# Kernel tuning notes

Measured on AMD Instinct MI355X. Metric: run time of the kernel, lower is better.

Reference implementation:

```python
import jax, jax.numpy as jnp
import numpy as np
from jax import lax

HIDDEN = 64


def setup_inputs() -> dict:
    key = jax.random.key(0)
    ks = jax.random.split(key, 8)
    B, T, C, H, W = 8, 16, 3, 64, 64
    x = jax.random.normal(ks[0], (B, T, C, H, W), dtype=jnp.float32)
    # SE-style attention 1x1 convs (no bias): fc1 3->1, fc2 1->3
    att_w1 = jax.random.normal(ks[1], (1, 3), dtype=jnp.float32) * 0.5
    att_w2 = jax.random.normal(ks[2], (3, 1), dtype=jnp.float32) * 0.5
    # ConvLSTM layer 0: in = 3 + 64 = 67, out = 4*64 gates, 3x3 kernel
    conv_w0 = jax.random.normal(ks[3], (4 * HIDDEN, 3 + HIDDEN, 3, 3), dtype=jnp.float32) * 0.05
    conv_b0 = jnp.zeros((4 * HIDDEN,), dtype=jnp.float32)
    # ConvLSTM layer 1: in = 64 + 64 = 128
    conv_w1 = jax.random.normal(ks[4], (4 * HIDDEN, 2 * HIDDEN, 3, 3), dtype=jnp.float32) * 0.05
    conv_b1 = jnp.zeros((4 * HIDDEN,), dtype=jnp.float32)
    return {"x": x, "att_w1": att_w1, "att_w2": att_w2,
            "conv_w0": conv_w0, "conv_b0": conv_b0,
            "conv_w1": conv_w1, "conv_b1": conv_b1}


def _attention_scale(x, w1, w2):
    # x: [B, T, C, H, W] -> channel attention per timestep, vectorized over B,T
    avg = x.mean(axis=(-2, -1))          # [B, T, C]
    mx = x.max(axis=(-2, -1))            # [B, T, C]
    def fc(v):
        return jnp.einsum('or,btr->bto', w2, jax.nn.relu(jnp.einsum('rc,btc->btr', w1, v)))
    return jax.nn.sigmoid(fc(avg) + fc(mx))  # [B, T, C]


def _convlstm_layer(xseq, w, b, hidden):
    # xseq: [B, T, Cin, H, W]; returns ([B, T, hidden, H, W], h_last, c_last)
    B, T, Cin, H, W = xseq.shape
    h0 = jnp.zeros((B, hidden, H, W), xseq.dtype)
    c0 = jnp.zeros((B, hidden, H, W), xseq.dtype)

    def step(carry, xt):
        h, c = carry
        comb = jnp.concatenate([xt, h], axis=1)  # [B, Cin+hidden, H, W]
        conv = lax.conv_general_dilated(
            comb, w, window_strides=(1, 1), padding='SAME',
            dimension_numbers=('NCHW', 'OIHW', 'NCHW')) + b[None, :, None, None]
        cc_i, cc_f, cc_o, cc_g = jnp.split(conv, 4, axis=1)
        c_new = jax.nn.sigmoid(cc_f) * c + jax.nn.sigmoid(cc_i) * jnp.tanh(cc_g)
        h_new = jax.nn.sigmoid(cc_o) * jnp.tanh(c_new)
        return (h_new, c_new), h_new

    (h_last, c_last), hs = lax.scan(step, (h0, c0), jnp.moveaxis(xseq, 1, 0))
    return jnp.moveaxis(hs, 0, 1), h_last, c_last


def reference(x, att_w1, att_w2, conv_w0, conv_b0, conv_w1, conv_b1):
    # attention gating (broadcast [B,T,C,1,1] over H,W as in torch broadcast assign)
    scale = _attention_scale(x, att_w1, att_w2)
    xin = x * scale[..., None, None]
    out0, _, _ = _convlstm_layer(xin, conv_w0, conv_b0, HIDDEN)
    out1, h1, c1 = _convlstm_layer(out0, conv_w1, conv_b1, HIDDEN)
    # return_all_layers=False: last layer output + its final state
    return out1, h1, c1
```

## Files before the change

kernel.cpp:

```cpp
#include <hip/hip_runtime.h>
#include <hip/hip_bf16.h>
#include <math.h>

#define HW 4096
#define NB 8
#define NT 16

typedef unsigned short u16;
typedef __attribute__((ext_vector_type(8))) short bf16x8;
typedef __attribute__((ext_vector_type(4))) float f32x4;

__device__ __forceinline__ float sigmoid_f(float x) {
  return 1.f / (1.f + __expf(-x));
}
__device__ __forceinline__ float tanh_f(float x) {
  float ax = fabsf(x);
  float e = __expf(2.f * ax);
  float t = 1.f - 2.f / (e + 1.f);
  return copysignf(t, x);
}
__device__ __forceinline__ u16 f2b(float v) {
  __hip_bfloat16 h = __float2bfloat16(v);
  return *(u16*)&h;
}

__global__ void transform_wB(const float* __restrict__ w, u16* __restrict__ wtB,
                             int CIN, int cinbase, int nch) {
  int idx = blockIdx.x * 256 + threadIdx.x;
  int total = nch * 9 * 256 * 32;
  if (idx >= total) return;
  int ci32 = idx & 31;
  int rest = idx >> 5;
  int gate = rest & 255;
  rest >>= 8;
  int tap = rest % 9;
  int chunk = rest / 9;
  int cin = cinbase + chunk * 32 + ci32;
  wtB[idx] = f2b(w[((size_t)gate * CIN + cin) * 9 + tap]);
}

__global__ void transform_wA(const float* __restrict__ w0, u16* __restrict__ wtA) {
  int idx = blockIdx.x * 256 + threadIdx.x;
  if (idx >= 8192) return;
  int k = idx & 31, gate = idx >> 5;
  u16 v = 0;
  if (k < 27) {
    int ci = (k >= 18) + (k >= 9);
    int tap = k - ci * 9;
    v = f2b(w0[((size_t)gate * 67 + ci) * 9 + tap]);
  }
  wtA[idx] = v;
}

__global__ void att_reduce(const float* __restrict__ x, float* __restrict__ avg,
                           float* __restrict__ mx) {
  int btc = blockIdx.x;
  const float* p = x + (size_t)btc * HW;
  float s = 0.f, m = -INFINITY;
  for (int i = threadIdx.x; i < HW; i += 256) {
    float v = p[i];
    s += v;
    m = fmaxf(m, v);
  }
  #pragma unroll
  for (int off = 32; off; off >>= 1) {
    s += __shfl_down(s, off, 64);
    m = fmaxf(m, __shfl_down(m, off, 64));
  }
  __shared__ float ss[4], sm[4];
  int wid = threadIdx.x >> 6, lane = threadIdx.x & 63;
  if (lane == 0) { ss[wid] = s; sm[wid] = m; }
  __syncthreads();
  if (threadIdx.x == 0) {
    avg[btc] = (ss[0] + ss[1] + ss[2] + ss[3]) * (1.f / 4096.f);
    mx[btc]  = fmaxf(fmaxf(sm[0], sm[1]), fmaxf(sm[2], sm[3]));
  }
}

__global__ void att_apply(const float* __restrict__ x, const float* __restrict__ avg,
                          const float* __restrict__ mx, const float* __restrict__ w1,
                          const float* __restrict__ w2, u16* __restrict__ xin_t) {
  size_t i = (size_t)blockIdx.x * 256 + threadIdx.x;
  int pix = (int)(i & 4095);
  int c   = (int)((i >> 12) % 3);
  int bt  = (int)(i / (3 * HW));
  const float* a = avg + bt * 3;
  const float* m = mx + bt * 3;
  float ra = fmaxf(0.f, w1[0] * a[0] + w1[1] * a[1] + w1[2] * a[2]);
  float rm = fmaxf(0.f, w1[0] * m[0] + w1[1] * m[1] + w1[2] * m[2]);
  float sc = sigmoid_f(w2[c] * (ra + rm));
  xin_t[((size_t)bt * HW + pix) * 4 + c] = f2b(x[i] * sc);
}

struct RoleP {
  const u16* a0; long a0_bs; const u16* wtA;
  const u16* s0; long s0_bs; int s0_ch;
  const u16* s1; long s1_bs; int s1_ch;
  const u16* wtB; const float* bias;
  float* c_t;
  u16* h_t;
  float* out_f32; long out_bs;
};

__device__ __forceinline__ void dma_site(const u16* sp, u16* bufn, int idx,
                                         const u16* zb, int r0g) {
  int site = idx >> 2, sub = idx & 3;
  int r = site / 66, cc = site - r * 66;
  int gr = r0g - 1 + r, gc = cc - 1;
  const u16* g = (site < 264 && (unsigned)gr < 64u && (unsigned)gc < 64u)
               ? sp + (size_t)(gr * 64 + gc) * 32 + sub * 8
               : zb;
  u16* l = bufn + (size_t)(idx & ~63) * 8;
  __builtin_amdgcn_global_load_lds(
      (const __attribute__((address_space(1))) unsigned int*)g,
      (__attribute__((address_space(3))) unsigned int*)l, 16, 0, 0);
}

__device__ __forceinline__ void dma_chunk(const u16* sp, u16* bufn, const u16* zb,
                                          int r0g, int tid) {
  #pragma unroll
  for (int it = 0; it < 4; ++it) dma_site(sp, bufn, it * 256 + tid, zb, r0g);
  if (tid < 64) dma_site(sp, bufn, 1024 + tid, zb, r0g);
}

#define BQ_LOAD(S, BASE, TP)                                              \
  { _Pragma("unroll")                                                     \
    for (int _g = 0; _g < 4; ++_g)                                        \
      bq[S][_g] = *(const bf16x8*)((BASE) + (TP) * 8192 + _g * 2048); }

template <int PAR>
__device__ __forceinline__ void chunk_compute(const u16* bufc, const u16* bpc,
                                              const u16* bpn, bool more,
                                              bf16x8 (&bq)[2][4], f32x4 (&acc)[8][4],
                                              int abase) {
  #pragma unroll
  for (int tap = 0; tap < 9; ++tap) {
    if (tap < 8) { BQ_LOAD((tap + 1 + PAR) & 1, bpc, tap + 1) }
    else if (more) { BQ_LOAD((1 + PAR) & 1, bpn, 0) }
    const int dy = tap / 3, dx = tap - dy * 3;
    bf16x8 av[8];
    #pragma unroll
    for (int mt = 0; mt < 8; ++mt)
      av[mt] = *(const bf16x8*)(bufc + abase + ((mt >> 2) + dy) * 2112 + dx * 32 + (mt & 3) * 512);
    #pragma unroll
    for (int mt = 0; mt < 8; ++mt)
      #pragma unroll
      for (int gt = 0; gt < 4; ++gt)
        acc[mt][gt] = __builtin_amdgcn_mfma_f32_16x16x32_bf16(
            av[mt], bq[(tap + PAR) & 1][gt], acc[mt][gt], 0, 0, 0);
  }
}

#define SP_SET(CG)                                                           \
  sp = ((CG) < P.s0_ch)                                                      \
     ? P.s0 + (size_t)b * P.s0_bs + (size_t)(CG) * 131072                    \
     : P.s1 + (size_t)b * P.s1_bs + (size_t)((CG) - P.s0_ch) * 131072;

__global__ __launch_bounds__(256, 2) void conv_step(
    RoleP r0p, RoleP r1p, int zbase, const u16* __restrict__ zb)
{
  __shared__ __align__(16) u16 smem[2][8704];
  __shared__ __align__(16) u16 xtile[4096];
  const RoleP P = (blockIdx.z + zbase) ? r1p : r0p;
  const int r0g = blockIdx.x * 2, b = blockIdx.y;
  const int tid = threadIdx.x;
  const int gc = tid >> 6, lane = tid & 63;
  const int n = lane & 15, q = lane >> 4;
  const int abase = n * 32 + q * 8;
  const int ntot = P.s0_ch + P.s1_ch;

  f32x4 acc[8][4];
  #pragma unroll
  for (int mt = 0; mt < 8; ++mt)
    #pragma unroll
    for (int gt = 0; gt < 4; ++gt)
      acc[mt][gt] = (f32x4){0.f, 0.f, 0.f, 0.f};

  const u16* bp0 = P.wtB + (size_t)(gc * 16 + n) * 32 + q * 8;
  bf16x8 bq[2][4];
  const u16* sp;

  SP_SET(0);
  dma_chunk(sp, &smem[0][0], zb, r0g, tid);
  BQ_LOAD(0, bp0, 0)
  if (P.a0) {
    const u16* ap = P.a0 + (size_t)b * P.a0_bs;
    for (int idx = tid; idx < 4096; idx += 256) {
      int row = idx >> 11, rest = idx & 2047;
      int k = rest & 31, px = rest >> 5;
      u16 v = 0;
      if (k < 27) {
        int ci = (k >= 18) + (k >= 9);
        int tap = k - ci * 9;
        int dy = (tap >= 6) ? 2 : (tap >= 3 ? 1 : 0);
        int dx = tap - dy * 3;
        int gr = r0g + row - 1 + dy, gcl = px - 1 + dx;
        if ((unsigned)gr < 64u && (unsigned)gcl < 64u)
          v = ap[((size_t)(gr * 64 + gcl)) * 4 + ci];
      }
      xtile[idx] = v;
    }
  }
  __syncthreads();
  if (P.a0) {
    bf16x8 bxa[4], axv[8];
    #pragma unroll
    for (int gt = 0; gt < 4; ++gt)
      bxa[gt] = *(const bf16x8*)(P.wtA + ((gc + 4 * gt) * 16 + n) * 32 + q * 8);
    #pragma unroll
    for (int mt = 0; mt < 8; ++mt)
      axv[mt] = *(const bf16x8*)(xtile + (mt >> 2) * 2048 + ((mt & 3) * 16 + n) * 32 + q * 8);
    #pragma unroll
    for (int mt = 0; mt < 8; ++mt)
      #pragma unroll
      for (int gt = 0; gt < 4; ++gt)
        acc[mt][gt] = __builtin_amdgcn_mfma_f32_16x16x32_bf16(axv[mt], bxa[gt], acc[mt][gt], 0, 0, 0);
  }

  int cur = 0;
  for (int cg = 0; cg < ntot; cg += 2) {
    {
      SP_SET(cg + 1);
      dma_chunk(sp, &smem[cur ^ 1][0], zb, r0g, tid);
      chunk_compute<0>(&smem[cur][0], bp0 + (size_t)cg * 73728,
                       bp0 + (size_t)(cg + 1) * 73728, true, bq, acc, abase);
      __syncthreads();
      cur ^= 1;
    }
    {
      bool more = (cg + 2 < ntot);
      if (more) {
        SP_SET(cg + 2);
        dma_chunk(sp, &smem[cur ^ 1][0], zb, r0g, tid);
      }
      chunk_compute<1>(&smem[cur][0], bp0 + (size_t)(cg + 1) * 73728,
                       bp0 + (size_t)(cg + 2) * 73728, more, bq, acc, abase);
      __syncthreads();
      cur ^= 1;
    }
  }

  const int hc = gc * 16 + n;
  const float bi = P.bias[hc], bfv = P.bias[64 + hc], bo = P.bias[128 + hc], bg = P.bias[192 + hc];
  float* cB = P.c_t + ((size_t)b * HW + r0g * 64) * 64 + hc;
  u16*   hB = P.h_t + (size_t)b * 262144 + (size_t)(hc >> 5) * 131072
            + (size_t)(r0g * 64) * 32 + (hc & 31);
  float* tbuf = (float*)&smem[0][0];
  #pragma unroll
  for (int mt = 0; mt < 8; ++mt) {
    #pragma unroll
    for (int reg = 0; reg < 4; ++reg) {
      int px = mt * 16 + q * 4 + reg;
      float xi = acc[mt][0][reg] + bi;
      float xf = acc[mt][1][reg] + bfv;
      float xo = acc[mt][2][reg] + bo;
      float xg = acc[mt][3][reg] + bg;
      float ii = sigmoid_f(xi), ff = sigmoid_f(xf), oo = sigmoid_f(xo), gg = tanh_f(xg);
      float cold = cB[(size_t)px * 64];
      float cnew = ff * cold + ii * gg;
      float hnew = oo * tanh_f(cnew);
      cB[(size_t)px * 64] = cnew;
      hB[(size_t)px * 32] = f2b(hnew);
      if (P.out_f32) tbuf[px * 65 + hc] = hnew;
    }
  }
  if (P.out_f32) {
    __syncthreads();
    int hc2 = tid >> 2, qq = tid & 3;
    #pragma unroll
    for (int rw = 0; rw < 2; ++rw) {
      float* orow = P.out_f32 + (size_t)b * P.out_bs + (size_t)hc2 * HW + (r0g + rw) * 64;
      #pragma unroll
      for (int j = 0; j < 4; ++j) {
        int p0x = qq * 4 + j * 16;
        float4 v = make_float4(tbuf[(rw * 64 + p0x + 0) * 65 + hc2],
                               tbuf[(rw * 64 + p0x + 1) * 65 + hc2],
                               tbuf[(rw * 64 + p0x + 2) * 65 + hc2],
                               tbuf[(rw * 64 + p0x + 3) * 65 + hc2]);
        *(float4*)(orow + p0x) = v;
      }
    }
  }
}

__global__ void h1_final(const float* __restrict__ out1, float* __restrict__ dst) {
  size_t i = (size_t)blockIdx.x * 256 + threadIdx.x;
  size_t b = i >> 18, rem = i & 262143;
  dst[i] = out1[(b * NT + (NT - 1)) * 262144 + rem];
}

__global__ void c1_final(const float* __restrict__ c_t, float* __restrict__ dst) {
  __shared__ float t[64][65];
  int pb = blockIdx.x, b = blockIdx.y;
  int tx = threadIdx.x & 63, ty = threadIdx.x >> 6;
  for (int i = 0; i < 16; ++i) {
    int p = i * 4 + ty;
    t[p][tx] = c_t[((size_t)b * HW + pb * 64 + p) * 64 + tx];
  }
  __syncthreads();
  for (int i = 0; i < 16; ++i) {
    int hcv = i * 4 + ty;
    dst[(size_t)b * 262144 + (size_t)hcv * HW + pb * 64 + tx] = t[tx][hcv];
  }
}

extern "C" void kernel_launch(void* const* d_in, const int* in_sizes, int n_in,
                              void* d_out, int out_size, void* d_ws, size_t ws_size,
                              hipStream_t stream) {
  const float* x      = (const float*)d_in[0];
  const float* att_w1 = (const float*)d_in[1];
  const float* att_w2 = (const float*)d_in[2];
  const float* w0     = (const float*)d_in[3];
  const float* b0     = (const float*)d_in[4];
  const float* w1     = (const float*)d_in[5];
  const float* b1     = (const float*)d_in[6];
  float* out = (float*)d_out;
  char* ws = (char*)d_ws;

  u16*   xin_t = (u16*)(ws + 0);
  u16*   h0a   = (u16*)(ws + 4194304);
  u16*   h0b   = (u16*)(ws + 8388608);
  u16*   h1a   = (u16*)(ws + 12582912);
  u16*   h1b   = (u16*)(ws + 16777216);
  u16*   zb    = (u16*)(ws + 20971520);
  u16*   wtA0  = (u16*)(ws + 21495808);
  u16*   wtB0  = (u16*)(ws + 21512192);
  u16*   wtB1  = (u16*)(ws + 21807104);
  float* c0_t  = (float*)(ws + 22396928);
  float* c1_t  = (float*)(ws + 30785536);
  float* avg   = (float*)(ws + 39174144);
  float* mxb   = (float*)(ws + 39175680);
  if (ws_size < 39177216u) return;

  hipMemsetAsync(xin_t, 0, 4194304, stream);
  hipMemsetAsync(zb, 0, 524288, stream);
  hipMemsetAsync(c0_t, 0, 8388608, stream);
  hipMemsetAsync(c1_t, 0, 8388608, stream);

  transform_wA<<<32, 256, 0, stream>>>(w0, wtA0);
  transform_wB<<<576, 256, 0, stream>>>(w0, wtB0, 67, 3, 2);
  transform_wB<<<1152, 256, 0, stream>>>(w1, wtB1, 128, 0, 4);
  att_reduce<<<NB * NT * 3, 256, 0, stream>>>(x, avg, mxb);
  att_apply<<<1572864 / 256, 256, 0, stream>>>(x, avg, mxb, att_w1, att_w2, xin_t);

  const long HB = 262144;

  for (int s = 0; s <= NT; ++s) {
    bool has0 = (s < NT), has1 = (s > 0);
    RoleP p0 = {}, p1 = {};
    if (has0) {
      int t = s;
      p0.a0 = xin_t + (size_t)t * 16384; p0.a0_bs = (long)NT * 16384; p0.wtA = wtA0;
      p0.s0 = (t == 0) ? zb : ((t & 1) ? h0a : h0b);
      p0.s0_bs = (t == 0) ? 0L : HB; p0.s0_ch = 2;
      p0.s1 = zb; p0.s1_bs = 0L; p0.s1_ch = 0;
      p0.wtB = wtB0; p0.bias = b0; p0.c_t = c0_t;
      p0.h_t = (t & 1) ? h0b : h0a;
      p0.out_f32 = (float*)0; p0.out_bs = 0L;
    }
    if (has1) {
      int t = s - 1;
      p1.a0 = (const u16*)0; p1.a0_bs = 0L; p1.wtA = (const u16*)0;
      p1.s0 = (t & 1) ? h0b : h0a;
      p1.s0_bs = HB; p1.s0_ch = 2;
      p1.s1 = (t == 0) ? zb : ((t & 1) ? h1a : h1b);
      p1.s1_bs = (t == 0) ? 0L : HB; p1.s1_ch = 2;
      p1.wtB = wtB1; p1.bias = b1; p1.c_t = c1_t;
      p1.h_t = (t & 1) ? h1b : h1a;
      p1.out_f32 = out + (size_t)t * 262144; p1.out_bs = (long)NT * 262144;
    }
    int zbase = has0 ? 0 : 1;
    int zn = (has0 && has1) ? 2 : 1;
    conv_step<<<dim3(32, 8, zn), 256, 0, stream>>>(p0, p1, zbase, zb);
  }

  h1_final<<<8192, 256, 0, stream>>>(out, out + 33554432);
  c1_final<<<dim3(64, 8), 256, 0, stream>>>(c1_t, out + 35651584);
}
```

Measured before the change: 914.9 us.

## Replace per-step conv launches with a persistent kernel and grid barrier

The 17 separate conv_step launches, one per wavefront step of the two-layer ConvLSTM, are replaced by a single persistent kernel of 512 blocks. Each block keeps a fixed role (layer 0 or layer 1) and spatial tile, and the blocks synchronise between steps with an atomic-counter grid barrier. This is meant to remove kernel launch and drain gaps between steps. The barrier relies on all 512 blocks being co-resident (2 blocks per CU at 256 CUs), and its spin loop has a timeout that could silently break synchronisation.

```diff
diff --git a/kernel.cpp b/kernel.cpp
--- a/kernel.cpp
+++ b/kernel.cpp
@@ -5,6 +5,8 @@
 #define HW 4096
 #define NB 8
 #define NT 16
+#define HB 262144L
+#define NBLK 512
 
 typedef unsigned short u16;
 typedef __attribute__((ext_vector_type(8))) short bf16x8;
@@ -102,6 +104,14 @@
   float* out_f32; long out_bs;
 };
 
+struct PP {
+  const u16* xin; const u16* wtA;
+  const u16* wtB0; const float* b0; float* c0; u16* h0a; u16* h0b;
+  const u16* wtB1; const float* b1; float* c1; u16* h1a; u16* h1b;
+  const u16* zb; float* out;
+  unsigned* bar;
+};
+
 __device__ __forceinline__ void dma_site(const u16* sp, u16* bufn, int idx,
                                          const u16* zb, int r0g) {
   int site = idx >> 2, sub = idx & 3;
@@ -156,14 +166,9 @@
      ? P.s0 + (size_t)b * P.s0_bs + (size_t)(CG) * 131072                    \
      : P.s1 + (size_t)b * P.s1_bs + (size_t)((CG) - P.s0_ch) * 131072;
 
-__global__ __launch_bounds__(256, 2) void conv_step(
-    RoleP r0p, RoleP r1p, int zbase, const u16* __restrict__ zb)
-{
-  __shared__ __align__(16) u16 smem[2][8704];
-  __shared__ __align__(16) u16 xtile[4096];
-  const RoleP P = (blockIdx.z + zbase) ? r1p : r0p;
-  const int r0g = blockIdx.x * 2, b = blockIdx.y;
-  const int tid = threadIdx.x;
+__device__ __forceinline__ void conv_body(const RoleP& P, const u16* zb,
+                                          u16 (&smem)[2][8704], u16 (&xtile)[4096],
+                                          int r0g, int b, int tid) {
   const int gc = tid >> 6, lane = tid & 63;
   const int n = lane & 15, q = lane >> 4;
   const int abase = n * 32 + q * 8;
@@ -283,6 +288,65 @@
   }
 }
 
+__device__ __forceinline__ void grid_barrier(unsigned* bar, unsigned step) {
+  __syncthreads();
+  if (threadIdx.x == 0) {
+    __threadfence();
+    unsigned old = __hip_atomic_fetch_add(&bar[0], 1u, __ATOMIC_ACQ_REL,
+                                          __HIP_MEMORY_SCOPE_AGENT);
+    if (old == NBLK - 1u) {
+      __hip_atomic_store(&bar[0], 0u, __ATOMIC_RELAXED, __HIP_MEMORY_SCOPE_AGENT);
+      __hip_atomic_store(&bar[1], step + 1u, __ATOMIC_RELEASE, __HIP_MEMORY_SCOPE_AGENT);
+    } else {
+      long spins = 0;
+      while (__hip_atomic_load(&bar[1], __ATOMIC_ACQUIRE,
+                               __HIP_MEMORY_SCOPE_AGENT) <= step) {
+        __builtin_amdgcn_s_sleep(2);
+        if (++spins > 2000000L) break;
+      }
+    }
+    __threadfence();
+  }
+  __syncthreads();
+}
+
+__global__ __launch_bounds__(256, 2) void conv_persist(PP pp) {
+  __shared__ __align__(16) u16 smem[2][8704];
+  __shared__ __align__(16) u16 xtile[4096];
+  const int bid = blockIdx.x;
+  const int role = bid & 1, tile = bid >> 1;
+  const int r0g = (tile & 31) * 2, b = tile >> 5;
+  const int tid = threadIdx.x;
+
+  for (int s = 0; s <= NT; ++s) {
+    const bool active = role ? (s > 0) : (s < NT);
+    if (active) {
+      const int t = role ? (s - 1) : s;
+      RoleP P;
+      if (!role) {
+        P.a0 = pp.xin + (size_t)t * 16384; P.a0_bs = (long)NT * 16384; P.wtA = pp.wtA;
+        P.s0 = (t == 0) ? pp.zb : ((t & 1) ? pp.h0a : pp.h0b);
+        P.s0_bs = (t == 0) ? 0L : HB; P.s0_ch = 2;
+        P.s1 = pp.zb; P.s1_bs = 0L; P.s1_ch = 0;
+        P.wtB = pp.wtB0; P.bias = pp.b0; P.c_t = pp.c0;
+        P.h_t = (t & 1) ? pp.h0b : pp.h0a;
+        P.out_f32 = (float*)0; P.out_bs = 0L;
+      } else {
+        P.a0 = (const u16*)0; P.a0_bs = 0L; P.wtA = (const u16*)0;
+        P.s0 = (t & 1) ? pp.h0b : pp.h0a;
+        P.s0_bs = HB; P.s0_ch = 2;
+        P.s1 = (t == 0) ? pp.zb : ((t & 1) ? pp.h1a : pp.h1b);
+        P.s1_bs = (t == 0) ? 0L : HB; P.s1_ch = 2;
+        P.wtB = pp.wtB1; P.bias = pp.b1; P.c_t = pp.c1;
+        P.h_t = (t & 1) ? pp.h1b : pp.h1a;
+        P.out_f32 = pp.out + (size_t)t * 262144; P.out_bs = (long)NT * 262144;
+      }
+      conv_body(P, pp.zb, smem, xtile, r0g, b, tid);
+    }
+    if (s < NT) grid_barrier(pp.bar, (unsigned)s);
+  }
+}
+
 __global__ void h1_final(const float* __restrict__ out1, float* __restrict__ dst) {
   size_t i = (size_t)blockIdx.x * 256 + threadIdx.x;
   size_t b = i >> 18, rem = i & 262143;
@@ -330,12 +394,14 @@
   float* c1_t  = (float*)(ws + 30785536);
   float* avg   = (float*)(ws + 39174144);
   float* mxb   = (float*)(ws + 39175680);
-  if (ws_size < 39177216u) return;
+  unsigned* bar = (unsigned*)(ws + 39177216);
+  if (ws_size < 39177280u) return;
 
   hipMemsetAsync(xin_t, 0, 4194304, stream);
   hipMemsetAsync(zb, 0, 524288, stream);
   hipMemsetAsync(c0_t, 0, 8388608, stream);
   hipMemsetAsync(c1_t, 0, 8388608, stream);
+  hipMemsetAsync(bar, 0, 64, stream);
 
   transform_wA<<<32, 256, 0, stream>>>(w0, wtA0);
   transform_wB<<<576, 256, 0, stream>>>(w0, wtB0, 67, 3, 2);
@@ -343,36 +409,12 @@
   att_reduce<<<NB * NT * 3, 256, 0, stream>>>(x, avg, mxb);
   att_apply<<<1572864 / 256, 256, 0, stream>>>(x, avg, mxb, att_w1, att_w2, xin_t);
 
-  const long HB = 262144;
-
-  for (int s = 0; s <= NT; ++s) {
-    bool has0 = (s < NT), has1 = (s > 0);
-    RoleP p0 = {}, p1 = {};
-    if (has0) {
-      int t = s;
-      p0.a0 = xin_t + (size_t)t * 16384; p0.a0_bs = (long)NT * 16384; p0.wtA = wtA0;
-      p0.s0 = (t == 0) ? zb : ((t & 1) ? h0a : h0b);
-      p0.s0_bs = (t == 0) ? 0L : HB; p0.s0_ch = 2;
-      p0.s1 = zb; p0.s1_bs = 0L; p0.s1_ch = 0;
-      p0.wtB = wtB0; p0.bias = b0; p0.c_t = c0_t;
-      p0.h_t = (t & 1) ? h0b : h0a;
-      p0.out_f32 = (float*)0; p0.out_bs = 0L;
-    }
-    if (has1) {
-      int t = s - 1;
-      p1.a0 = (const u16*)0; p1.a0_bs = 0L; p1.wtA = (const u16*)0;
-      p1.s0 = (t & 1) ? h0b : h0a;
-      p1.s0_bs = HB; p1.s0_ch = 2;
-      p1.s1 = (t == 0) ? zb : ((t & 1) ? h1a : h1b);
-      p1.s1_bs = (t == 0) ? 0L : HB; p1.s1_ch = 2;
-      p1.wtB = wtB1; p1.bias = b1; p1.c_t = c1_t;
-      p1.h_t = (t & 1) ? h1b : h1a;
-      p1.out_f32 = out + (size_t)t * 262144; p1.out_bs = (long)NT * 262144;
-    }
-    int zbase = has0 ? 0 : 1;
-    int zn = (has0 && has1) ? 2 : 1;
-    conv_step<<<dim3(32, 8, zn), 256, 0, stream>>>(p0, p1, zbase, zb);
-  }
+  PP pp;
+  pp.xin = xin_t; pp.wtA = wtA0;
+  pp.wtB0 = wtB0; pp.b0 = b0; pp.c0 = c0_t; pp.h0a = h0a; pp.h0b = h0b;
+  pp.wtB1 = wtB1; pp.b1 = b1; pp.c1 = c1_t; pp.h1a = h1a; pp.h1b = h1b;
+  pp.zb = zb; pp.out = out; pp.bar = bar;
+  conv_persist<<<NBLK, 256, 0, stream>>>(pp);
 
   h1_final<<<8192, 256, 0, stream>>>(out, out + 33554432);
   c1_final<<<dim3(64, 8), 256, 0, stream>>>(c1_t, out + 35651584);
```

New measurement: 3.015 ms. 230% more time.
